# Optimization experiments

Hardware: AMD Instinct MI355X
Metric: run time of the kernel (lower is better)

The kernel has to match this reference:

```python
import jax, jax.numpy as jnp
import numpy as np

N_NODES = 40000
N_EDGES = 640000
N_GRAPHS = 64
F_IN = 32       # fourier_order*4
D_EMB = 256     # int(0.5*512)
D_HID = 512     # int(0.5*1024)
D_FC = 1024     # int(0.5*2048)
N_CLS = 10


def setup_inputs() -> dict:
    key = jax.random.key(0)
    ks = iter(jax.random.split(key, 40))
    rn = lambda shape, s=0.05: jax.random.normal(next(ks), shape, jnp.float32) * s
    inp = {
        'x': jax.random.normal(next(ks), (N_NODES, F_IN), jnp.float32),
        'edge_index': jax.random.randint(next(ks), (2, N_EDGES), 0, N_NODES, jnp.int32),
        'edge_attr': jax.random.uniform(next(ks), (N_EDGES, 1), jnp.float32),
        'batch': jnp.sort(jax.random.randint(next(ks), (N_NODES,), 0, N_GRAPHS, jnp.int32)),
        # embedding MLP
        'emb_w1': rn((F_IN, D_EMB)), 'emb_b1': jnp.zeros((D_EMB,), jnp.float32),
        'emb_w2': rn((D_EMB, D_EMB)), 'emb_b2': jnp.zeros((D_EMB,), jnp.float32),
        # edge_proj MLP
        'ep_w1': rn((1, 64)), 'ep_b1': jnp.zeros((64,), jnp.float32),
        'ep_w2': rn((64, 1)), 'ep_b2': jnp.zeros((1,), jnp.float32),
        # GCNConv weights (x @ W + b, PyG convention)
        'w_c1': rn((D_EMB, D_HID)), 'b_c1': jnp.zeros((D_HID,), jnp.float32),
        'w_c2': rn((D_HID, D_HID)), 'b_c2': jnp.zeros((D_HID,), jnp.float32),
        'w_c3': rn((D_HID, D_HID)), 'b_c3': jnp.zeros((D_HID,), jnp.float32),
        'w_c4': rn((D_HID, D_HID)), 'b_c4': jnp.zeros((D_HID,), jnp.float32),
        'w_c5': rn((D_HID, D_HID)), 'b_c5': jnp.zeros((D_HID,), jnp.float32),
        'w_c6': rn((D_HID, D_HID)), 'b_c6': jnp.zeros((D_HID,), jnp.float32),
        # head
        'fc1_w': rn((D_HID, D_FC)), 'fc1_b': jnp.zeros((D_FC,), jnp.float32),
        'head_w': rn((D_FC, N_CLS)), 'head_b': jnp.zeros((N_CLS,), jnp.float32),
    }
    return inp


def _gcn_conv(x, src, dst, norm, W, b):
    # PyG GCNConv: linear transform, then normalized scatter-add aggregation, then bias
    h = x @ W                                   # [N, d_out]
    msg = h[src] * norm[:, None]                # [E+N, d_out] gathered messages
    agg = jax.ops.segment_sum(msg, dst, num_segments=N_NODES)
    return agg + b


def _forward(x, edge_attr, emb_w1, emb_b1, emb_w2, emb_b2, ep_w1, ep_b1, ep_w2, ep_b2,
             w_c1, b_c1, w_c2, b_c2, w_c3, b_c3, w_c4, b_c4, w_c5, b_c5, w_c6, b_c6,
             fc1_w, fc1_b, head_w, head_b, edge_index, batch):
    # edge weights from edge_proj MLP (sigmoid output in (0,1))
    ew = jax.nn.sigmoid(jax.nn.relu(edge_attr @ ep_w1 + ep_b1) @ ep_w2 + ep_b2)[:, 0]  # [E]
    # gcn_norm with self loops (identical for every conv layer -> compute once)
    loops = jnp.arange(N_NODES, dtype=edge_index.dtype)
    src = jnp.concatenate([edge_index[0], loops])
    dst = jnp.concatenate([edge_index[1], loops])
    w = jnp.concatenate([ew, jnp.ones((N_NODES,), ew.dtype)])
    deg = jax.ops.segment_sum(w, dst, num_segments=N_NODES)
    dinv = jnp.where(deg > 0, jax.lax.rsqrt(jnp.maximum(deg, 1e-12)), 0.0)
    norm = dinv[src] * w * dinv[dst]            # [E+N]

    h = jax.nn.relu(jax.nn.relu(x @ emb_w1 + emb_b1) @ emb_w2 + emb_b2)
    h = _gcn_conv(h, src, dst, norm, w_c1, b_c1)
    skip = jax.nn.relu(h)
    h = _gcn_conv(skip, src, dst, norm, w_c2, b_c2)
    h = jax.nn.relu(h)
    h = _gcn_conv(h, src, dst, norm, w_c3, b_c3)
    skip = jax.nn.relu(h) + skip                # has_skip=True
    h = _gcn_conv(skip, src, dst, norm, w_c4, b_c4)  # is_deep=True
    h = jax.nn.relu(h)
    h = _gcn_conv(h, src, dst, norm, w_c5, b_c5)
    h = jax.nn.relu(h)
    h = _gcn_conv(h, src, dst, norm, w_c6, b_c6)
    skip = jax.nn.relu(h) + skip

    # global mean pool over graphs
    sums = jax.ops.segment_sum(skip, batch, num_segments=N_GRAPHS)
    cnts = jax.ops.segment_sum(jnp.ones((N_NODES,), skip.dtype), batch, num_segments=N_GRAPHS)
    pooled = sums / jnp.maximum(cnts, 1.0)[:, None]   # [G, D_HID]

    out = jax.nn.relu(pooled @ fc1_w + fc1_b) @ head_w + head_b   # [G, N_CLS]
    return out


def reference(x, edge_index, edge_attr, batch, emb_w1, emb_b1, emb_w2, emb_b2,
              ep_w1, ep_b1, ep_w2, ep_b2, w_c1, b_c1, w_c2, b_c2, w_c3, b_c3,
              w_c4, b_c4, w_c5, b_c5, w_c6, b_c6, fc1_w, fc1_b, head_w, head_b):
    return _forward(x, edge_attr, emb_w1, emb_b1, emb_w2, emb_b2, ep_w1, ep_b1, ep_w2, ep_b2,
                    w_c1, b_c1, w_c2, b_c2, w_c3, b_c3, w_c4, b_c4, w_c5, b_c5, w_c6, b_c6,
                    fc1_w, fc1_b, head_w, head_b, edge_index, batch)
```

## Files before the change

### kernel.cpp

```cpp
#include <hip/hip_runtime.h>
#include <math.h>

#define N_NODES 40000
#define MP      40192
#define NROWB   157
#define N_EDGES 640000
#define N_GRAPHS 64
#define F_IN 32
#define D_EMB 256
#define D_HID 512
#define D_FC 1024
#define N_CLS 10

typedef _Float16 f16x8 __attribute__((ext_vector_type(8)));
typedef float f32x4  __attribute__((ext_vector_type(4)));
typedef unsigned short u16;

template <int N> struct VecU;
template <> struct VecU<2> { typedef unsigned T __attribute__((ext_vector_type(2))); };
template <> struct VecU<4> { typedef unsigned T __attribute__((ext_vector_type(4))); };

__device__ __forceinline__ float h2f(u16 u) {
    union { u16 s; _Float16 h; } v; v.s = u; return (float)v.h;
}
__device__ __forceinline__ u16 f2h(float f) {
    union { u16 s; _Float16 h; } v; v.h = (_Float16)f; return v.s;
}
__device__ __forceinline__ void async16(void* lds, const void* g) {
    __builtin_amdgcn_global_load_lds((const __attribute__((address_space(1))) void*)g,
                                     (__attribute__((address_space(3))) void*)lds, 16, 0, 0);
}

__global__ void prep_all(const float* __restrict__ x, u16* __restrict__ xb, u16* __restrict__ G,
                         float* __restrict__ deg, int* __restrict__ cnt, int* __restrict__ cursor,
                         float* __restrict__ sums) {
    int i = blockIdx.x * blockDim.x + threadIdx.x;
    if (i < N_NODES) { deg[i] = 1.0f; cnt[i] = 0; cursor[i] = 0; }
    if (i < MP * F_IN) {
        int row = i >> 5;
        xb[i] = (row < N_NODES) ? f2h(x[i]) : (u16)0;
    }
    if (i < (MP - N_NODES) * D_HID) G[(size_t)N_NODES * D_HID + i] = 0;
    if (i < N_GRAPHS * D_HID) sums[i] = 0.f;
}

__global__ void edge_mlp_deg(const float* __restrict__ edge_attr,
                             const float* __restrict__ ep_w1, const float* __restrict__ ep_b1,
                             const float* __restrict__ ep_w2, const float* __restrict__ ep_b2,
                             const int* __restrict__ dst,
                             float* __restrict__ ew, float* __restrict__ deg, int* __restrict__ cnt) {
    __shared__ float w1[64], b1[64], w2[64];
    int t = threadIdx.x;
    if (t < 64) { w1[t] = ep_w1[t]; b1[t] = ep_b1[t]; w2[t] = ep_w2[t]; }
    __syncthreads();
    int e = blockIdx.x * blockDim.x + t;
    if (e >= N_EDGES) return;
    float x = edge_attr[e];
    float s = ep_b2[0];
#pragma unroll
    for (int j = 0; j < 64; ++j) s += fmaxf(x * w1[j] + b1[j], 0.f) * w2[j];
    float sig = 1.f / (1.f + expf(-s));
    ew[e] = sig;
    int d = dst[e];
    atomicAdd(&deg[d], sig);
    atomicAdd(&cnt[d], 1);
}

__global__ void dinv_kernel(const float* __restrict__ deg, float* __restrict__ dinv,
                            float* __restrict__ nloop) {
    int i = blockIdx.x * blockDim.x + threadIdx.x;
    if (i >= N_NODES) return;
    float d = deg[i];
    float r = (d > 0.f) ? rsqrtf(fmaxf(d, 1e-12f)) : 0.f;
    dinv[i] = r;
    nloop[i] = r * r;
}

__global__ void scan_kernel(const int* __restrict__ cnt, int* __restrict__ rowptr) {
    __shared__ int part[1024];
    int t = threadIdx.x;
    const int PER = (N_NODES + 1023) / 1024;
    int base = t * PER;
    int s = 0;
    for (int k = 0; k < PER; ++k) { int i = base + k; if (i < N_NODES) s += cnt[i]; }
    part[t] = s;
    __syncthreads();
    for (int off = 1; off < 1024; off <<= 1) {
        int v = (t >= off) ? part[t - off] : 0;
        __syncthreads();
        part[t] += v;
        __syncthreads();
    }
    int run = (t == 0) ? 0 : part[t - 1];
    for (int k = 0; k < PER; ++k) {
        int i = base + k;
        if (i < N_NODES) { rowptr[i] = run; run += cnt[i]; }
    }
    if (t == 1023) rowptr[N_NODES] = run;
}

__global__ void fill_csr_kernel(const int* __restrict__ src, const int* __restrict__ dst,
                                const float* __restrict__ ew, const float* __restrict__ dinv,
                                const int* __restrict__ rowptr, int* __restrict__ cursor,
                                int2* __restrict__ cv) {
    int e = blockIdx.x * blockDim.x + threadIdx.x;
    if (e >= N_EDGES) return;
    int d = dst[e];
    int s = src[e];
    float n = dinv[s] * ew[e] * dinv[d];
    int p = rowptr[d] + atomicAdd(&cursor[d], 1);
    cv[p] = make_int2(s, __float_as_int(n));
}

struct WPair { const float* s; u16* d; int K; int N; };
struct WP8 { WPair m[8]; };

__global__ void wprep_all(WP8 a) {
    __shared__ u16 th[32][33];
    WPair w = a.m[blockIdx.z];
    int n0 = blockIdx.x * 32;
    int k0 = blockIdx.y * 32;
    if (n0 >= w.N || k0 >= w.K) return;
    int tx = threadIdx.x, ty = threadIdx.y;
#pragma unroll
    for (int r = 0; r < 4; ++r) {
        int k = ty + r * 8;
        th[k][tx] = f2h(w.s[(size_t)(k0 + k) * w.N + n0 + tx]);
    }
    __syncthreads();
#pragma unroll
    for (int r = 0; r < 4; ++r) {
        int n = ty + r * 8;
        w.d[(size_t)(n0 + n) * w.K + k0 + tx] = th[tx][n];
    }
}

__launch_bounds__(512)
__global__ void mfma_gemm(const u16* __restrict__ A,
                          const u16* __restrict__ W,
                          const float* __restrict__ bias,
                          const u16* __restrict__ skip,
                          u16* __restrict__ C, int K, int N,
                          const int* __restrict__ batch, float* __restrict__ pool) {
    __shared__ __align__(16) u16 smem[2 * 12288];
    __shared__ int sbatch[128];

    int nColB = N >> 7;
    int b = blockIdx.x;
    int rowI = (b >> 3) / nColB * 8 + (b & 7);
    int colI = (b >> 3) % nColB;
    if (rowI >= NROWB) return;
    int rowBase = rowI * 256;
    int colBase = colI * 128;

    int t = threadIdx.x;
    int lane = t & 63;
    int wave = t >> 6;
    int wr = wave >> 1;
    int wc = wave & 1;

    int tt  = (lane & 7) ^ ((lane >> 3) & 7);
    int rrl = ((lane >> 3) << 1) | (tt >> 2);
    int sel = (tt & 3) * 8;
    int r0A = wave * 32;
    int r0W = wave * 16;

    int quad = lane >> 4;
    int mrow = lane & 15;

    const u16* gA = A + (size_t)(rowBase + r0A + rrl) * K + sel;
    const u16* gW = W + (size_t)(colBase + r0W + rrl) * K + sel;

    f32x4 acc[4][4] = {};

    int nIter = K >> 5;
    {
        u16* As = smem; u16* Ws = smem + 8192;
        async16(&As[r0A * 32], gA);
        async16(&As[(r0A + 16) * 32], gA + (size_t)16 * K);
        async16(&Ws[r0W * 32], gW);
    }

    for (int it = 0; it < nIter; ++it) {
        int cur = it & 1;
        __builtin_amdgcn_s_barrier();
        if (it + 1 < nIter) {
            int k0 = (it + 1) << 5;
            u16* As = smem + (cur ^ 1) * 12288; u16* Ws = As + 8192;
            async16(&As[r0A * 32], gA + k0);
            async16(&As[(r0A + 16) * 32], gA + k0 + (size_t)16 * K);
            async16(&Ws[r0W * 32], gW + k0);
            asm volatile("s_waitcnt vmcnt(3)" ::: "memory");
        } else {
            asm volatile("s_waitcnt vmcnt(0)" ::: "memory");
        }
        __builtin_amdgcn_sched_barrier(0);
        __builtin_amdgcn_s_barrier();
        __builtin_amdgcn_sched_barrier(0);

        const u16* As = smem + cur * 12288;
        const u16* Ws = As + 8192;
        f16x8 af[4], wf[4];
#pragma unroll
        for (int i = 0; i < 4; ++i) {
            int Ra = wr * 64 + i * 16 + mrow;
            int sa = ((Ra & 1) * 4 + quad) ^ ((Ra >> 1) & 7);
            af[i] = *(const f16x8*)&As[(Ra >> 1) * 64 + sa * 8];
            int Rb = wc * 64 + i * 16 + mrow;
            int sb = ((Rb & 1) * 4 + quad) ^ ((Rb >> 1) & 7);
            wf[i] = *(const f16x8*)&Ws[(Rb >> 1) * 64 + sb * 8];
        }
#pragma unroll
        for (int i = 0; i < 4; ++i)
#pragma unroll
            for (int j = 0; j < 4; ++j)
                acc[i][j] = __builtin_amdgcn_mfma_f32_16x16x32_f16(af[i], wf[j], acc[i][j], 0, 0, 0);
    }
    __syncthreads();

    const int ES = 132;
    u16* eb = smem;
#pragma unroll
    for (int ph = 0; ph < 2; ++ph) {
        if ((wr >> 1) == ph) {
#pragma unroll
            for (int j = 0; j < 4; ++j) {
                int col = colBase + wc * 64 + j * 16 + mrow;
                float bv = bias[col];
#pragma unroll
                for (int i = 0; i < 4; ++i) {
#pragma unroll
                    for (int r = 0; r < 4; ++r) {
                        int lr = (wr & 1) * 64 + i * 16 + quad * 4 + r;
                        size_t row = (size_t)rowBase + ph * 128 + lr;
                        float v = fmaxf(acc[i][j][r] + bv, 0.f);
                        if (skip) v += h2f(skip[row * N + col]);
                        eb[lr * ES + wc * 64 + j * 16 + mrow] = f2h(v);
                    }
                }
            }
        }
        if (pool && t < 128) {
            int row = rowBase + ph * 128 + t;
            sbatch[t] = (row < N_NODES) ? batch[row] : -1;
        }
        __syncthreads();
        if (C) {
#pragma unroll
            for (int k = 0; k < 4; ++k) {
                int c = t + k * 512;
                int row = c >> 4;
                int ch = c & 15;
                f16x8 v = *(const f16x8*)&eb[row * ES + ch * 8];
                *(f16x8*)&C[(size_t)(rowBase + ph * 128 + row) * N + colBase + ch * 8] = v;
            }
        }
        if (pool) {
            int c = t & 127;
            int rs = (t >> 7) * 32;
            float run = 0.f; int g = -1;
            for (int r = rs; r < rs + 32; ++r) {
                int bg = sbatch[r];
                if (bg != g) {
                    if (g >= 0) atomicAdd(&pool[(size_t)g * D_HID + colBase + c], run);
                    run = 0.f; g = bg;
                }
                if (bg >= 0) run += h2f(eb[r * ES + c]);
            }
            if (g >= 0) atomicAdd(&pool[(size_t)g * D_HID + colBase + c], run);
        }
        __syncthreads();
    }
}

template <int D>
__launch_bounds__(256)
__global__ void gather_f16(const u16* __restrict__ h, const int* __restrict__ rowptr,
                           const int2* __restrict__ cv, const float* __restrict__ nloop,
                           u16* __restrict__ out) {
    constexpr int FPL = D / 64;
    constexpr int UPL = FPL / 2;
    using VU = typename VecU<UPL>::T;
    int node = blockIdx.x * 4 + (threadIdx.x >> 6);
    int lane = threadIdx.x & 63;
    if (node >= N_NODES) return;
    union UU { unsigned u; _Float16 h[2]; };
    float acc[FPL];
    float sl = nloop[node];
    {
        VU own = *(const VU*)(h + (size_t)node * D + lane * FPL);
#pragma unroll
        for (int u = 0; u < UPL; ++u) {
            UU w; w.u = own[u];
            acc[2 * u]     = (float)w.h[0] * sl;
            acc[2 * u + 1] = (float)w.h[1] * sl;
        }
    }
    int beg = rowptr[node], end = rowptr[node + 1];
    if (end > beg) {
        int last = end - 1;
        int2 c[8];
#pragma unroll
        for (int m = 0; m < 8; ++m) c[m] = cv[min(beg + m, last)];
        for (int j = beg; j < end; j += 8) {
            VU tv[8];
#pragma unroll
            for (int m = 0; m < 8; ++m)
                tv[m] = *(const VU*)(h + (size_t)c[m].x * D + lane * FPL);
            int jn = j + 8;
            int2 cn[8];
#pragma unroll
            for (int m = 0; m < 8; ++m) cn[m] = c[m];
            if (jn < end) {
#pragma unroll
                for (int m = 0; m < 8; ++m) cn[m] = cv[min(jn + m, last)];
            }
            __builtin_amdgcn_sched_barrier(0);
#pragma unroll
            for (int m = 0; m < 8; ++m) {
                float v = (j + m < end) ? __int_as_float(c[m].y) : 0.f;
#pragma unroll
                for (int u = 0; u < UPL; ++u) {
                    UU w; w.u = tv[m][u];
                    acc[2 * u]     += (float)w.h[0] * v;
                    acc[2 * u + 1] += (float)w.h[1] * v;
                }
            }
#pragma unroll
            for (int m = 0; m < 8; ++m) c[m] = cn[m];
        }
    }
    VU o;
#pragma unroll
    for (int u = 0; u < UPL; ++u) {
        unsigned lo = f2h(acc[2 * u]);
        unsigned hi = f2h(acc[2 * u + 1]);
        o[u] = lo | (hi << 16);
    }
    *(VU*)(out + (size_t)node * D + lane * FPL) = o;
}

__launch_bounds__(1024)
__global__ void fc1_head(const float* __restrict__ sums, const int* __restrict__ batch,
                         const float* __restrict__ fc1_w, const float* __restrict__ fc1_b,
                         const float* __restrict__ head_w, const float* __restrict__ head_b,
                         float* __restrict__ out) {
    __shared__ float sv[D_HID];
    __shared__ float hacc[N_CLS];
    __shared__ float invc;
    int g = blockIdx.x;
    int t = threadIdx.x;
    if (t == 0) {
        int lo = 0, hi = N_NODES;
        while (lo < hi) { int m = (lo + hi) >> 1; if (batch[m] < g) lo = m + 1; else hi = m; }
        int lb = lo;
        lo = lb; hi = N_NODES;
        while (lo < hi) { int m = (lo + hi) >> 1; if (batch[m] < g + 1) lo = m + 1; else hi = m; }
        invc = 1.f / fmaxf((float)(lo - lb), 1.f);
    }
    if (t < N_CLS) hacc[t] = 0.f;
    __syncthreads();
    if (t < D_HID) sv[t] = sums[(size_t)g * D_HID + t] * invc;
    __syncthreads();
    int j = t;
    float acc = fc1_b[j];
#pragma unroll 8
    for (int k = 0; k < D_HID; ++k) acc += sv[k] * fc1_w[(size_t)k * D_FC + j];
    float f = fmaxf(acc, 0.f);
    float p[N_CLS];
#pragma unroll
    for (int c = 0; c < N_CLS; ++c) p[c] = f * head_w[j * N_CLS + c];
#pragma unroll
    for (int c = 0; c < N_CLS; ++c) {
        float v = p[c];
        for (int off = 32; off; off >>= 1) v += __shfl_down(v, off, 64);
        if ((t & 63) == 0) atomicAdd(&hacc[c], v);
    }
    __syncthreads();
    if (t < N_CLS) out[g * N_CLS + t] = hacc[t] + head_b[t];
}

extern "C" void kernel_launch(void* const* d_in, const int* in_sizes, int n_in,
                              void* d_out, int out_size, void* d_ws, size_t ws_size,
                              hipStream_t stream) {
    const float* x          = (const float*)d_in[0];
    const int*   edge_index = (const int*)d_in[1];
    const float* edge_attr  = (const float*)d_in[2];
    const int*   batch      = (const int*)d_in[3];
    const float* emb_w1 = (const float*)d_in[4];
    const float* emb_b1 = (const float*)d_in[5];
    const float* emb_w2 = (const float*)d_in[6];
    const float* emb_b2 = (const float*)d_in[7];
    const float* ep_w1  = (const float*)d_in[8];
    const float* ep_b1  = (const float*)d_in[9];
    const float* ep_w2  = (const float*)d_in[10];
    const float* ep_b2  = (const float*)d_in[11];
    const float* w_c[6] = { (const float*)d_in[12], (const float*)d_in[14], (const float*)d_in[16],
                            (const float*)d_in[18], (const float*)d_in[20], (const float*)d_in[22] };
    const float* b_c[6] = { (const float*)d_in[13], (const float*)d_in[15], (const float*)d_in[17],
                            (const float*)d_in[19], (const float*)d_in[21], (const float*)d_in[23] };
    const float* fc1_w  = (const float*)d_in[24];
    const float* fc1_b  = (const float*)d_in[25];
    const float* head_w = (const float*)d_in[26];
    const float* head_b = (const float*)d_in[27];
    float* out = (float*)d_out;

    const int* src = edge_index;
    const int* dst = edge_index + N_EDGES;

    char* p = (char*)d_ws;
    auto alloc = [&](size_t bytes) { char* r = p; p += (bytes + 255) & ~(size_t)255; return r; };
    float* ew    = (float*)alloc(N_EDGES * 4);
    float* deg   = (float*)alloc(N_NODES * 4);
    float* dinv  = (float*)alloc(N_NODES * 4);
    float* nloop = (float*)alloc(N_NODES * 4);
    int* cnt     = (int*)alloc(N_NODES * 4);
    int* cursor  = (int*)alloc(N_NODES * 4);
    int* rowptr  = (int*)alloc((N_NODES + 1) * 4);
    int2* cv     = (int2*)alloc((size_t)N_EDGES * 8);
    u16* xb = (u16*)alloc((size_t)MP * F_IN * 2);
    u16* H1 = (u16*)alloc((size_t)MP * D_EMB * 2);
    u16* H2 = (u16*)alloc((size_t)MP * D_EMB * 2);
    u16* G  = (u16*)alloc((size_t)MP * D_HID * 2);
    u16* S1 = (u16*)alloc((size_t)MP * D_HID * 2);
    u16* S2 = (u16*)alloc((size_t)MP * D_HID * 2);
    u16* Cb = (u16*)alloc((size_t)MP * D_HID * 2);
    u16* we1 = (u16*)alloc((size_t)F_IN * D_EMB * 2);
    u16* we2 = (u16*)alloc((size_t)D_EMB * D_EMB * 2);
    u16* wc[6];
    wc[0] = (u16*)alloc((size_t)D_EMB * D_HID * 2);
    for (int i = 1; i < 6; ++i) wc[i] = (u16*)alloc((size_t)D_HID * D_HID * 2);
    float* sums = (float*)alloc(N_GRAPHS * D_HID * 4);

    const int TB = 256;
    const int EB = (N_EDGES + TB - 1) / TB;
    const int NB = (N_NODES + TB - 1) / TB;

    prep_all<<<(MP * F_IN + TB - 1) / TB, TB, 0, stream>>>(x, xb, G, deg, cnt, cursor, sums);
    edge_mlp_deg<<<EB, TB, 0, stream>>>(edge_attr, ep_w1, ep_b1, ep_w2, ep_b2, dst, ew, deg, cnt);
    dinv_kernel<<<NB, TB, 0, stream>>>(deg, dinv, nloop);
    scan_kernel<<<1, 1024, 0, stream>>>(cnt, rowptr);
    fill_csr_kernel<<<EB, TB, 0, stream>>>(src, dst, ew, dinv, rowptr, cursor, cv);

    WP8 wp;
    wp.m[0] = { emb_w1, we1, F_IN,  D_EMB };
    wp.m[1] = { emb_w2, we2, D_EMB, D_EMB };
    wp.m[2] = { w_c[0], wc[0], D_EMB, D_HID };
    for (int i = 1; i < 6; ++i) wp.m[2 + i] = { w_c[i], wc[i], D_HID, D_HID };
    wprep_all<<<dim3(16, 16, 8), dim3(32, 8), 0, stream>>>(wp);

    const int SLOTS = ((NROWB + 7) / 8) * 8;
    const int GRID2 = SLOTS * (D_EMB / 128);
    const int GRID4 = SLOTS * (D_HID / 128);
    mfma_gemm<<<GRID2, 512, 0, stream>>>(xb, we1, emb_b1, nullptr, H1, F_IN, D_EMB, nullptr, nullptr);
    mfma_gemm<<<GRID2, 512, 0, stream>>>(H1, we2, emb_b2, nullptr, H2, D_EMB, D_EMB, nullptr, nullptr);

    const int GG = (N_NODES + 3) / 4;
    gather_f16<D_EMB><<<GG, 256, 0, stream>>>(H2, rowptr, cv, nloop, G);
    mfma_gemm<<<GRID4, 512, 0, stream>>>(G, wc[0], b_c[0], nullptr, S1, D_EMB, D_HID, nullptr, nullptr);
    gather_f16<D_HID><<<GG, 256, 0, stream>>>(S1, rowptr, cv, nloop, G);
    mfma_gemm<<<GRID4, 512, 0, stream>>>(G, wc[1], b_c[1], nullptr, Cb, D_HID, D_HID, nullptr, nullptr);
    gather_f16<D_HID><<<GG, 256, 0, stream>>>(Cb, rowptr, cv, nloop, G);
    mfma_gemm<<<GRID4, 512, 0, stream>>>(G, wc[2], b_c[2], S1, S2, D_HID, D_HID, nullptr, nullptr);
    gather_f16<D_HID><<<GG, 256, 0, stream>>>(S2, rowptr, cv, nloop, G);
    mfma_gemm<<<GRID4, 512, 0, stream>>>(G, wc[3], b_c[3], nullptr, Cb, D_HID, D_HID, nullptr, nullptr);
    gather_f16<D_HID><<<GG, 256, 0, stream>>>(Cb, rowptr, cv, nloop, G);
    mfma_gemm<<<GRID4, 512, 0, stream>>>(G, wc[4], b_c[4], nullptr, Cb, D_HID, D_HID, nullptr, nullptr);
    gather_f16<D_HID><<<GG, 256, 0, stream>>>(Cb, rowptr, cv, nloop, G);
    mfma_gemm<<<GRID4, 512, 0, stream>>>(G, wc[5], b_c[5], S2, nullptr, D_HID, D_HID, batch, sums);

    fc1_head<<<N_GRAPHS, 1024, 0, stream>>>(sums, batch, fc1_w, fc1_b, head_w, head_b, out);
}
```

Measured before the change: 1.203 ms.

## Pre-pack GEMM operands into swizzled tile-contiguous layout for contiguous async loads

The A and W operands of the MFMA GEMM are now stored in a blocked, pre-swizzled layout that matches the LDS tile image. Each async 16-byte load per k-step then reads one contiguous chunk instead of strided rows. The weight prep, input conversion, gather output and the first embedding GEMM write this packed format, and a new packed-output path feeds the second GEMM. The intent is to improve global-load coalescing and DRAM locality in the GEMMs, at the cost of scattered stores in the producers and a layout that must stay consistent across every kernel.

Result: no change. 1.206 ms (+0.2%).

```diff
diff --git a/kernel.cpp b/kernel.cpp
--- a/kernel.cpp
+++ b/kernel.cpp
@@ -31,16 +31,31 @@
                                      (__attribute__((address_space(3))) void*)lds, 16, 0, 0);
 }
 
+__device__ __forceinline__ int pk_idx(int r, int q) {
+    int rp = r >> 1;
+    int g  = (((r & 1) << 2) | q) ^ (rp & 7);
+    return rp * 64 + g * 8;
+}
+
 __global__ void prep_all(const float* __restrict__ x, u16* __restrict__ xb, u16* __restrict__ G,
                          float* __restrict__ deg, int* __restrict__ cnt, int* __restrict__ cursor,
                          float* __restrict__ sums) {
     int i = blockIdx.x * blockDim.x + threadIdx.x;
     if (i < N_NODES) { deg[i] = 1.0f; cnt[i] = 0; cursor[i] = 0; }
     if (i < MP * F_IN) {
-        int row = i >> 5;
-        xb[i] = (row < N_NODES) ? f2h(x[i]) : (u16)0;
-    }
-    if (i < (MP - N_NODES) * D_HID) G[(size_t)N_NODES * D_HID + i] = 0;
+        int row = i >> 5, colk = i & 31;
+        float v = (row < N_NODES) ? x[i] : 0.f;
+        size_t idx = (size_t)(row >> 8) * 8192 + pk_idx(row & 255, colk >> 3) + (colk & 7);
+        xb[idx] = f2h(v);
+    }
+    if (i < 16 * 3072) {
+        int kc = i / 3072, rem = i % 3072;
+        G[(size_t)(156 * 16 + kc) * 8192 + 5120 + rem] = 0;
+    } else if (i < 16 * 3072 + 8 * 3072) {
+        int j = i - 16 * 3072;
+        int kc = j / 3072, rem = j % 3072;
+        G[(size_t)(156 * 8 + kc) * 8192 + 5120 + rem] = 0;
+    }
     if (i < N_GRAPHS * D_HID) sums[i] = 0.f;
 }
 
@@ -131,7 +146,11 @@
 #pragma unroll
     for (int r = 0; r < 4; ++r) {
         int n = ty + r * 8;
-        w.d[(size_t)(n0 + n) * w.K + k0 + tx] = th[tx][n];
+        int R = n0 + n;
+        int kcol = k0 + tx;
+        size_t idx = ((size_t)(R >> 7) * (w.K >> 5) + (kcol >> 5)) * 4096
+                   + pk_idx(R & 127, (kcol >> 3) & 3) + (kcol & 7);
+        w.d[idx] = th[tx][n];
     }
 }
 
@@ -140,7 +159,8 @@
                           const u16* __restrict__ W,
                           const float* __restrict__ bias,
                           const u16* __restrict__ skip,
-                          u16* __restrict__ C, int K, int N,
+                          u16* __restrict__ C, u16* __restrict__ Cpk,
+                          int K, int N,
                           const int* __restrict__ batch, float* __restrict__ pool) {
     __shared__ __align__(16) u16 smem[2 * 12288];
     __shared__ int sbatch[128];
@@ -159,37 +179,32 @@
     int wr = wave >> 1;
     int wc = wave & 1;
 
-    int tt  = (lane & 7) ^ ((lane >> 3) & 7);
-    int rrl = ((lane >> 3) << 1) | (tt >> 2);
-    int sel = (tt & 3) * 8;
-    int r0A = wave * 32;
-    int r0W = wave * 16;
-
     int quad = lane >> 4;
     int mrow = lane & 15;
 
-    const u16* gA = A + (size_t)(rowBase + r0A + rrl) * K + sel;
-    const u16* gW = W + (size_t)(colBase + r0W + rrl) * K + sel;
+    const u16* pA = A + (size_t)rowI * (K >> 5) * 8192 + wave * 1024 + (lane << 3);
+    const u16* pW = W + (size_t)colI * (K >> 5) * 4096 + wave * 512 + (lane << 3);
 
     f32x4 acc[4][4] = {};
 
     int nIter = K >> 5;
     {
         u16* As = smem; u16* Ws = smem + 8192;
-        async16(&As[r0A * 32], gA);
-        async16(&As[(r0A + 16) * 32], gA + (size_t)16 * K);
-        async16(&Ws[r0W * 32], gW);
+        async16(&As[wave * 1024], pA);
+        async16(&As[wave * 1024 + 512], pA + 512);
+        async16(&Ws[wave * 512], pW);
     }
 
     for (int it = 0; it < nIter; ++it) {
         int cur = it & 1;
         __builtin_amdgcn_s_barrier();
         if (it + 1 < nIter) {
-            int k0 = (it + 1) << 5;
             u16* As = smem + (cur ^ 1) * 12288; u16* Ws = As + 8192;
-            async16(&As[r0A * 32], gA + k0);
-            async16(&As[(r0A + 16) * 32], gA + k0 + (size_t)16 * K);
-            async16(&Ws[r0W * 32], gW + k0);
+            const u16* sA = pA + (size_t)(it + 1) * 8192;
+            const u16* sW = pW + (size_t)(it + 1) * 4096;
+            async16(&As[wave * 1024], sA);
+            async16(&As[wave * 1024 + 512], sA + 512);
+            async16(&Ws[wave * 512], sW);
             asm volatile("s_waitcnt vmcnt(3)" ::: "memory");
         } else {
             asm volatile("s_waitcnt vmcnt(0)" ::: "memory");
@@ -247,12 +262,23 @@
         __syncthreads();
         if (C) {
 #pragma unroll
-            for (int k = 0; k < 4; ++k) {
-                int c = t + k * 512;
+            for (int k2 = 0; k2 < 4; ++k2) {
+                int c = t + k2 * 512;
                 int row = c >> 4;
                 int ch = c & 15;
                 f16x8 v = *(const f16x8*)&eb[row * ES + ch * 8];
                 *(f16x8*)&C[(size_t)(rowBase + ph * 128 + row) * N + colBase + ch * 8] = v;
+            }
+        } else if (Cpk) {
+#pragma unroll
+            for (int k2 = 0; k2 < 4; ++k2) {
+                int c = t + k2 * 512;
+                int row = c >> 4;
+                int ch = c & 15;
+                f16x8 v = *(const f16x8*)&eb[row * ES + ch * 8];
+                size_t idx = ((size_t)rowI * (N >> 5) + (colBase >> 5) + (ch >> 2)) * 8192
+                           + pk_idx(ph * 128 + row, ch & 3);
+                *(f16x8*)&Cpk[idx] = v;
             }
         }
         if (pool) {
@@ -337,7 +363,15 @@
         unsigned hi = f2h(acc[2 * u + 1]);
         o[u] = lo | (hi << 16);
     }
-    *(VU*)(out + (size_t)node * D + lane * FPL) = o;
+    size_t blkb = (size_t)(node >> 8) * (D >> 5);
+    int rr = node & 255;
+    if (D == 512) {
+        size_t idx = (blkb + (lane >> 2)) * 8192 + pk_idx(rr, lane & 3);
+        *(VU*)(out + idx) = o;
+    } else {
+        size_t idx = (blkb + (lane >> 3)) * 8192 + pk_idx(rr, (lane >> 1) & 3) + (lane & 1) * 4;
+        *(VU*)(out + idx) = o;
+    }
 }
 
 __launch_bounds__(1024)
@@ -452,22 +486,22 @@
     const int SLOTS = ((NROWB + 7) / 8) * 8;
     const int GRID2 = SLOTS * (D_EMB / 128);
     const int GRID4 = SLOTS * (D_HID / 128);
-    mfma_gemm<<<GRID2, 512, 0, stream>>>(xb, we1, emb_b1, nullptr, H1, F_IN, D_EMB, nullptr, nullptr);
-    mfma_gemm<<<GRID2, 512, 0, stream>>>(H1, we2, emb_b2, nullptr, H2, D_EMB, D_EMB, nullptr, nullptr);
+    mfma_gemm<<<GRID2, 512, 0, stream>>>(xb, we1, emb_b1, nullptr, nullptr, H1, F_IN, D_EMB, nullptr, nullptr);
+    mfma_gemm<<<GRID2, 512, 0, stream>>>(H1, we2, emb_b2, nullptr, H2, nullptr, D_EMB, D_EMB, nullptr, nullptr);
 
     const int GG = (N_NODES + 3) / 4;
     gather_f16<D_EMB><<<GG, 256, 0, stream>>>(H2, rowptr, cv, nloop, G);
-    mfma_gemm<<<GRID4, 512, 0, stream>>>(G, wc[0], b_c[0], nullptr, S1, D_EMB, D_HID, nullptr, nullptr);
+    mfma_gemm<<<GRID4, 512, 0, stream>>>(G, wc[0], b_c[0], nullptr, S1, nullptr, D_EMB, D_HID, nullptr, nullptr);
     gather_f16<D_HID><<<GG, 256, 0, stream>>>(S1, rowptr, cv, nloop, G);
-    mfma_gemm<<<GRID4, 512, 0, stream>>>(G, wc[1], b_c[1], nullptr, Cb, D_HID, D_HID, nullptr, nullptr);
+    mfma_gemm<<<GRID4, 512, 0, stream>>>(G, wc[1], b_c[1], nullptr, Cb, nullptr, D_HID, D_HID, nullptr, nullptr);
     gather_f16<D_HID><<<GG, 256, 0, stream>>>(Cb, rowptr, cv, nloop, G);
-    mfma_gemm<<<GRID4, 512, 0, stream>>>(G, wc[2], b_c[2], S1, S2, D_HID, D_HID, nullptr, nullptr);
+    mfma_gemm<<<GRID4, 512, 0, stream>>>(G, wc[2], b_c[2], S1, S2, nullptr, D_HID, D_HID, nullptr, nullptr);
     gather_f16<D_HID><<<GG, 256, 0, stream>>>(S2, rowptr, cv, nloop, G);
-    mfma_gemm<<<GRID4, 512, 0, stream>>>(G, wc[3], b_c[3], nullptr, Cb, D_HID, D_HID, nullptr, nullptr);
+    mfma_gemm<<<GRID4, 512, 0, stream>>>(G, wc[3], b_c[3], nullptr, Cb, nullptr, D_HID, D_HID, nullptr, nullptr);
     gather_f16<D_HID><<<GG, 256, 0, stream>>>(Cb, rowptr, cv, nloop, G);
-    mfma_gemm<<<GRID4, 512, 0, stream>>>(G, wc[4], b_c[4], nullptr, Cb, D_HID, D_HID, nullptr, nullptr);
+    mfma_gemm<<<GRID4, 512, 0, stream>>>(G, wc[4], b_c[4], nullptr, Cb, nullptr, D_HID, D_HID, nullptr, nullptr);
     gather_f16<D_HID><<<GG, 256, 0, stream>>>(Cb, rowptr, cv, nloop, G);
-    mfma_gemm<<<GRID4, 512, 0, stream>>>(G, wc[5], b_c[5], S2, nullptr, D_HID, D_HID, batch, sums);
+    mfma_gemm<<<GRID4, 512, 0, stream>>>(G, wc[5], b_c[5], S2, nullptr, nullptr, D_HID, D_HID, batch, sums);
 
     fc1_head<<<N_GRAPHS, 1024, 0, stream>>>(sums, batch, fc1_w, fc1_b, head_w, head_b, out);
 }
```
